# Optimization experiments

Measured on AMD Instinct MI355X. Metric: run time of the kernel, lower is better.

The kernel has to match this reference:

```python
import jax, jax.numpy as jnp
import numpy as np


def recursive_fht(x):
    # Faithful vectorized version of the module's recursive butterfly FHT
    # (twiddle = cas(2*pi*n/N), no flipped-odd term, exactly as in the source).
    N = x.shape[-1]
    if N == 1:
        return x
    e = recursive_fht(x[..., ::2])
    o = recursive_fht(x[..., 1::2])
    n = jnp.arange(N // 2, dtype=x.dtype)
    t = jnp.cos(2 * jnp.pi * n / N) + jnp.sin(2 * jnp.pi * n / N)
    return jnp.concatenate([e + t * o, e - t * o], axis=-1)


def compl_mul1d(x1, x2):
    # x1: [B, i, modes], x2: [i, o, modes]; flips along axis 0 as in the source
    x1f = x1[::-1]
    x2f = x2[::-1]
    return 0.5 * (jnp.einsum('bix,iox->box', x1, x2)
                  - jnp.einsum('bix,iox->box', x1f, x2f)
                  + jnp.einsum('bix,iox->box', x1, x2f)
                  + jnp.einsum('bix,iox->box', x1f, x2))


def idht(X):
    # Inverse discrete Hartley transform via the cas matrix (DHT is an
    # involution up to 1/K). K = N//2+1 is not a power of 2, so a dense
    # transform is used. Compute-bound batched GEMM.
    K = X.shape[-1]
    n = jnp.arange(K, dtype=X.dtype)
    ang = 2.0 * jnp.pi * jnp.outer(n, n) / K
    cas = jnp.cos(ang) + jnp.sin(ang)  # [K, K]
    return jnp.einsum('bck,kn->bcn', X, cas) / K


def setup_inputs() -> dict:
    key = jax.random.key(0)
    k1, k2 = jax.random.split(key)
    B, Cin, Cout, N, modes1 = 32, 64, 64, 4096, 1024
    x = jax.random.normal(k1, (B, Cin, N), dtype=jnp.float32)
    scale = 1.0 / (Cin * Cout)
    weights1 = scale * jax.random.uniform(k2, (Cin, Cout, modes1), dtype=jnp.float32)
    return {"x": x, "weights1": weights1, "modes1": modes1}


def reference(x, weights1, modes1):
    B, C, N = x.shape
    # dht with threshold=1.0: FHT along last axis, low-pass filter is a no-op
    x_ht = recursive_fht(x)
    K = N // 2 + 1
    out_ht = jnp.zeros((B, C, K), dtype=x.dtype)
    out_ht = out_ht.at[:, :, :modes1].set(compl_mul1d(x_ht[:, :, :modes1], weights1))
    return idht(out_ht)  # [B, C, N//2+1]
```

## Files before the change

kernel.cpp:

```cpp
#include <hip/hip_runtime.h>
#include <hip/hip_bf16.h>

#define BATCH 32
#define CIN   64
#define COUT  64
#define NFFT  4096
#define MODES 1024
#define KOUT  2049
#define NPAD  2176

typedef __bf16 bf16x8 __attribute__((ext_vector_type(8)));
typedef float  f32x4  __attribute__((ext_vector_type(4)));

#define AS1 __attribute__((address_space(1)))
#define AS3 __attribute__((address_space(3)))

static __device__ __forceinline__ void gl_lds16(const void* g, void* l) {
    __builtin_amdgcn_global_load_lds((const AS1 void*)g, (AS3 void*)l, 16, 0, 0);
}

static __device__ __forceinline__ void bfly4(float eA, float eB, float oA, float oB,
                                             float t, float c0, float c1,
                                             float& w0, float& w1, float& w2, float& w3) {
    float PA = fmaf(t, oA, eA), MA = fmaf(-t, oA, eA);
    float PB = fmaf(t, oB, eB), MB = fmaf(-t, oB, eB);
    w0 = fmaf(c0, PB, PA);
    w2 = fmaf(-c0, PB, PA);
    w1 = fmaf(c1, MB, MA);
    w3 = fmaf(-c1, MB, MA);
}


__global__ void fill_tw(float* __restrict__ tw) {
    int t = blockIdx.x * blockDim.x + threadIdx.x;
    if (t >= NFFT) return;
    if (t == 0) { tw[0] = 1.0f; return; }
    int h = 1 << (31 - __clz(t));
    int n = t - h;
    float ang = 3.14159265358979323846f * (float)n / (float)h;
    tw[t] = cosf(ang) + sinf(ang);
}

__global__ void fill_c2t(__hip_bfloat16* __restrict__ hi) {
    int idx = blockIdx.x * blockDim.x + threadIdx.x;
    if (idx >= NPAD * MODES) return;
    int n = idx >> 10;
    int k = idx & 1023;
    float v = 0.0f;
    if (n < KOUT) {
        int m = (k * n) % KOUT;
        float ang = 6.28318530717958647692f * (float)m / (float)KOUT;
        v = (cosf(ang) + sinf(ang)) * (1.0f / (float)KOUT);
    }
    hi[idx] = __float2bfloat16(v);
}

__global__ __launch_bounds__(256) void fht_kernel(const float* __restrict__ x,
                                                  const float* __restrict__ tw,
                                                  float* __restrict__ xh) {
    __shared__ float ldsA[4352];
    __shared__ float ldsB[4352];
    const int t = threadIdx.x;
    const int row = blockIdx.x;
    const float* xr = x + (size_t)row * NFFT;

    float r[4][4];
#pragma unroll
    for (int a = 0; a < 4; ++a)
#pragma unroll
        for (int c = 0; c < 4; ++c)
            r[a][c] = xr[t + 256 * a + 1024 * c];

    float o1[4][4];
#pragma unroll
    for (int a = 0; a < 4; ++a) {
        float PA = r[a][0] + r[a][2], MA = r[a][0] - r[a][2];
        float PB = r[a][1] + r[a][3], MB = r[a][1] - r[a][3];
        o1[a][0] = PA + PB;
        o1[a][2] = PA - PB;
        o1[a][1] = MA + MB;
        o1[a][3] = MA - MB;
    }
    float o2[4][4];
#pragma unroll
    for (int kap = 0; kap < 4; ++kap) {
        float tt = tw[4 + kap], c0 = tw[8 + kap], c1 = tw[12 + kap];
        bfly4(o1[0][kap], o1[1][kap], o1[2][kap], o1[3][kap], tt, c0, c1,
              o2[kap][0], o2[kap][1], o2[kap][2], o2[kap][3]);
    }
#pragma unroll
    for (int kap = 0; kap < 4; ++kap)
#pragma unroll
        for (int c = 0; c < 4; ++c) {
            int p = t + 256 * kap + 1024 * c;
            ldsA[p + (p >> 4)] = o2[kap][c];
        }
    __syncthreads();

    const int kap2 = t >> 4, gp = t & 15;
    float r2[4][4];
#pragma unroll
    for (int a = 0; a < 4; ++a)
#pragma unroll
        for (int c = 0; c < 4; ++c) {
            int p = 256 * kap2 + gp + 16 * a + 64 * c;
            r2[a][c] = ldsA[p + (p >> 4)];
        }
    float o3[4][4];
    {
        float tt = tw[16 + kap2], c0 = tw[32 + kap2], c1 = tw[48 + kap2];
#pragma unroll
        for (int a = 0; a < 4; ++a)
            bfly4(r2[a][0], r2[a][1], r2[a][2], r2[a][3], tt, c0, c1,
                  o3[a][0], o3[a][1], o3[a][2], o3[a][3]);
    }
    float o4[4][4];
#pragma unroll
    for (int c = 0; c < 4; ++c) {
        int kap3 = kap2 + 16 * c;
        float tt = tw[64 + kap3], c0 = tw[128 + kap3], c1 = tw[192 + kap3];
        bfly4(o3[0][c], o3[1][c], o3[2][c], o3[3][c], tt, c0, c1,
              o4[c][0], o4[c][1], o4[c][2], o4[c][3]);
    }
#pragma unroll
    for (int c = 0; c < 4; ++c)
#pragma unroll
        for (int cc = 0; cc < 4; ++cc) {
            int p = t + 256 * c + 1024 * cc;
            ldsB[p + (p >> 4)] = o4[c][cc];
        }
    __syncthreads();

    float r3[4][4];
#pragma unroll
    for (int g = 0; g < 4; ++g)
#pragma unroll
        for (int c = 0; c < 4; ++c) {
            int p = 16 * t + g + 4 * c;
            r3[g][c] = ldsB[p + (p >> 4)];
        }
    float o5[4][4];
    {
        float tt = tw[256 + t], c0 = tw[512 + t], c1 = tw[768 + t];
#pragma unroll
        for (int g = 0; g < 4; ++g)
            bfly4(r3[g][0], r3[g][1], r3[g][2], r3[g][3], tt, c0, c1,
                  o5[g][0], o5[g][1], o5[g][2], o5[g][3]);
    }
    float* xo = xh + (size_t)row * MODES;
#pragma unroll
    for (int c = 0; c < 4; ++c) {
        float tt = tw[1024 + t + 256 * c];
        float c0 = tw[2048 + t + 256 * c];
        float PA = fmaf(tt, o5[2][c], o5[0][c]);
        float PB = fmaf(tt, o5[3][c], o5[1][c]);
        xo[t + 256 * c] = fmaf(c0, PB, PA);
    }
}

__global__ __launch_bounds__(256) void mix_kernel(const f32x4* __restrict__ xh,
                                                  const f32x4* __restrict__ w,
                                                  ushort4* __restrict__ y_hi) {
    const int kl = threadIdx.x & 63;
    const int jg = threadIdx.x >> 6;
    const int k4 = blockIdx.x * 64 + kl;
    const int b  = blockIdx.y;
    const int rb = (BATCH - 1) - b;
    const int o  = blockIdx.z * 4 + jg;

    f32x4 accb = (f32x4){0.f, 0.f, 0.f, 0.f};
    f32x4 accr = (f32x4){0.f, 0.f, 0.f, 0.f};

#pragma unroll 4
    for (int i = 0; i < 32; ++i) {
        const int mi = 63 - i;
        f32x4 xai = xh[(size_t)(b  * CIN + i ) * 256 + k4];
        f32x4 xam = xh[(size_t)(b  * CIN + mi) * 256 + k4];
        f32x4 xbi = xh[(size_t)(rb * CIN + i ) * 256 + k4];
        f32x4 xbm = xh[(size_t)(rb * CIN + mi) * 256 + k4];
        f32x4 w1 = w[(size_t)(i  * COUT + o) * 256 + k4];
        f32x4 w2 = w[(size_t)(mi * COUT + o) * 256 + k4];
        f32x4 sa = xai + xam;
        f32x4 da = xai - xam;
        f32x4 sb = xbi + xbm;
        f32x4 db = xbi - xbm;
        f32x4 wp = w1 + w2, wm = w1 - w2;
        accb += sa * wp + db * wm;
        accr += sb * wp + da * wm;
    }

    const size_t ib = (size_t)(b  * COUT + o) * 256 + k4;
    const size_t ir = (size_t)(rb * COUT + o) * 256 + k4;
    f32x4 vb = accb * 0.5f;
    f32x4 vr = accr * 0.5f;
    __hip_bfloat16 b0 = __float2bfloat16(vb.x), b1 = __float2bfloat16(vb.y),
                   b2 = __float2bfloat16(vb.z), b3 = __float2bfloat16(vb.w);
    __hip_bfloat16 r0 = __float2bfloat16(vr.x), r1 = __float2bfloat16(vr.y),
                   r2 = __float2bfloat16(vr.z), r3 = __float2bfloat16(vr.w);
    y_hi[ib] = make_ushort4(*(unsigned short*)&b0, *(unsigned short*)&b1,
                            *(unsigned short*)&b2, *(unsigned short*)&b3);
    y_hi[ir] = make_ushort4(*(unsigned short*)&r0, *(unsigned short*)&r1,
                            *(unsigned short*)&r2, *(unsigned short*)&r3);
}

__global__ __launch_bounds__(256) void idht_mfma(const __hip_bfloat16* __restrict__ yh,
                                                 const __hip_bfloat16* __restrict__ ch,
                                                 float* __restrict__ out) {
    __shared__ __align__(16) char sa[2][8 * 1024];
    __shared__ __align__(16) char sb[2][4 * 1024];

    const int tid  = threadIdx.x;
    const int lane = tid & 63;
    const int wave = tid >> 6;
    const int wm = wave & 1;
    const int wn = wave >> 1;
    const int rbase = blockIdx.x * 128;
    const int nbase = blockIdx.y * 64;

    const int lrow = (lane & 15) * 2048;
    const int lchk = (lane >> 4) * 16;

    const char* ga  = (const char*)yh + (size_t)rbase * 2048;
    const char* gbh = (const char*)ch + (size_t)nbase * 2048;

    f32x4 acc[4][2];
#pragma unroll
    for (int mt = 0; mt < 4; ++mt)
#pragma unroll
        for (int nt = 0; nt < 2; ++nt) acc[mt][nt] = (f32x4){0.f, 0.f, 0.f, 0.f};

    auto stage = [&](int bi, int k0) {
#pragma unroll
        for (int r = 0; r < 2; ++r) {
            int g = wave + r * 4;
            gl_lds16(ga + (size_t)(g * 16) * 2048 + lrow + lchk + k0 * 2,
                     sa[bi] + g * 1024);
        }
        gl_lds16(gbh + (size_t)(wave * 16) * 2048 + lrow + lchk + k0 * 2,
                 sb[bi] + wave * 1024);
    };

    stage(0, 0);
    int cur = 0;
    for (int ks = 0; ks < MODES / 32; ++ks) {
        __syncthreads();
        if (ks + 1 < MODES / 32) stage(cur ^ 1, (ks + 1) * 32);
        bf16x8 a_[4], b_[2];
#pragma unroll
        for (int mt = 0; mt < 4; ++mt)
            a_[mt] = *(const bf16x8*)(sa[cur] + (wm * 4 + mt) * 1024 + lane * 16);
#pragma unroll
        for (int nt = 0; nt < 2; ++nt)
            b_[nt] = *(const bf16x8*)(sb[cur] + (wn * 2 + nt) * 1024 + lane * 16);
#pragma unroll
        for (int mt = 0; mt < 4; ++mt)
#pragma unroll
            for (int nt = 0; nt < 2; ++nt)
                acc[mt][nt] = __builtin_amdgcn_mfma_f32_16x16x32_bf16(a_[mt], b_[nt], acc[mt][nt], 0, 0, 0);
        cur ^= 1;
    }

#pragma unroll
    for (int mt = 0; mt < 4; ++mt) {
        int row = rbase + wm * 64 + mt * 16 + (lane >> 4) * 4;
#pragma unroll
        for (int nt = 0; nt < 2; ++nt) {
            int col = nbase + wn * 32 + nt * 16 + (lane & 15);
            if (col < KOUT) {
#pragma unroll
                for (int r = 0; r < 4; ++r)
                    out[(size_t)(row + r) * KOUT + col] = acc[mt][nt][r];
            }
        }
    }
}

extern "C" void kernel_launch(void* const* d_in, const int* in_sizes, int n_in,
                              void* d_out, int out_size, void* d_ws, size_t ws_size,
                              hipStream_t stream) {
    const float* x = (const float*)d_in[0];
    const float* w = (const float*)d_in[1];
    float* out = (float*)d_out;

    float* tw = (float*)d_ws;
    float* xh = tw + NFFT;
    __hip_bfloat16* y_hi = (__hip_bfloat16*)(xh + (size_t)BATCH * CIN * MODES);
    __hip_bfloat16* c2h  = y_hi + (size_t)BATCH * COUT * MODES;

    fill_tw<<<NFFT / 256, 256, 0, stream>>>(tw);
    fill_c2t<<<(NPAD * MODES + 255) / 256, 256, 0, stream>>>(c2h);
    fht_kernel<<<BATCH * CIN, 256, 0, stream>>>(x, tw, xh);
    mix_kernel<<<dim3(4, 16, 16), 256, 0, stream>>>((const f32x4*)xh, (const f32x4*)w,
                                                    (ushort4*)y_hi);
    idht_mfma<<<dim3((BATCH * COUT) / 128, NPAD / 64), 256, 0, stream>>>(y_hi, c2h, out);
}
```

Before: 161.0 us.

## Pre-swizzle cas table into MFMA fragment layout and load B directly to registers

The cas table is now written in a per-lane MFMA fragment order, so the idht kernel reads B straight from global memory into registers with one-step prefetch instead of staging it through LDS. The GEMM tile changes from 128x64 with 4 waves to 64x64 with 2 waves, and padding shrinks from 2176 to 2112 columns to cut wasted MFMA work. The two table-fill kernels are merged into one launch. In exchange, B is no longer shared through LDS between waves, so global/L2 traffic for the table rises and register pressure from the prefetch grows.

After: 154.0 us. -4.3%, faster.

```diff
diff --git a/kernel.cpp b/kernel.cpp
--- a/kernel.cpp
+++ b/kernel.cpp
@@ -7,7 +7,7 @@
 #define NFFT  4096
 #define MODES 1024
 #define KOUT  2049
-#define NPAD  2176
+#define NPAD  2112
 
 typedef __bf16 bf16x8 __attribute__((ext_vector_type(8)));
 typedef float  f32x4  __attribute__((ext_vector_type(4)));
@@ -30,29 +30,45 @@
     w3 = fmaf(-c1, MB, MA);
 }
 
-
-__global__ void fill_tw(float* __restrict__ tw) {
-    int t = blockIdx.x * blockDim.x + threadIdx.x;
-    if (t >= NFFT) return;
-    if (t == 0) { tw[0] = 1.0f; return; }
-    int h = 1 << (31 - __clz(t));
-    int n = t - h;
-    float ang = 3.14159265358979323846f * (float)n / (float)h;
-    tw[t] = cosf(ang) + sinf(ang);
-}
-
-__global__ void fill_c2t(__hip_bfloat16* __restrict__ hi) {
-    int idx = blockIdx.x * blockDim.x + threadIdx.x;
-    if (idx >= NPAD * MODES) return;
-    int n = idx >> 10;
-    int k = idx & 1023;
-    float v = 0.0f;
-    if (n < KOUT) {
-        int m = (k * n) % KOUT;
-        float ang = 6.28318530717958647692f * (float)m / (float)KOUT;
-        v = (cosf(ang) + sinf(ang)) * (1.0f / (float)KOUT);
-    }
-    hi[idx] = __float2bfloat16(v);
+#define NCHUNK ((NPAD / 16) * (MODES / 32) * 64)
+
+__global__ void fill_tables(float* __restrict__ tw, __hip_bfloat16* __restrict__ c2f) {
+    int gid = blockIdx.x * 256 + threadIdx.x;
+    if (gid < NCHUNK) {
+        int nl  = gid & 15;
+        int kc  = (gid >> 4) & 3;
+        int blk = gid >> 6;
+        int kb  = blk & 31;
+        int gn  = blk >> 5;
+        int n = gn * 16 + nl;
+        int kbase = kb * 32 + kc * 8;
+        unsigned short v8[8];
+        if (n < KOUT) {
+#pragma unroll
+            for (int j = 0; j < 8; ++j) {
+                int k = kbase + j;
+                int m = (k * n) % KOUT;
+                float ang = 6.28318530717958647692f * (float)m / (float)KOUT;
+                float v = (cosf(ang) + sinf(ang)) * (1.0f / (float)KOUT);
+                __hip_bfloat16 h = __float2bfloat16(v);
+                v8[j] = *(unsigned short*)&h;
+            }
+        } else {
+#pragma unroll
+            for (int j = 0; j < 8; ++j) v8[j] = 0;
+        }
+        *(ushort4*)((char*)c2f + (size_t)gid * 16)     = make_ushort4(v8[0], v8[1], v8[2], v8[3]);
+        *(ushort4*)((char*)c2f + (size_t)gid * 16 + 8) = make_ushort4(v8[4], v8[5], v8[6], v8[7]);
+    } else {
+        int t = gid - NCHUNK;
+        if (t < NFFT) {
+            if (t == 0) { tw[0] = 1.0f; return; }
+            int h = 1 << (31 - __clz(t));
+            int n = t - h;
+            float ang = 3.14159265358979323846f * (float)n / (float)h;
+            tw[t] = cosf(ang) + sinf(ang);
+        }
+    }
 }
 
 __global__ __launch_bounds__(256) void fht_kernel(const float* __restrict__ x,
@@ -203,69 +219,76 @@
                             *(unsigned short*)&r2, *(unsigned short*)&r3);
 }
 
-__global__ __launch_bounds__(256) void idht_mfma(const __hip_bfloat16* __restrict__ yh,
-                                                 const __hip_bfloat16* __restrict__ ch,
+__global__ __launch_bounds__(128) void idht_mfma(const __hip_bfloat16* __restrict__ yh,
+                                                 const __hip_bfloat16* __restrict__ c2f,
                                                  float* __restrict__ out) {
-    __shared__ __align__(16) char sa[2][8 * 1024];
-    __shared__ __align__(16) char sb[2][4 * 1024];
+    __shared__ __align__(16) char sa[2][4 * 1024];
 
     const int tid  = threadIdx.x;
     const int lane = tid & 63;
     const int wave = tid >> 6;
-    const int wm = wave & 1;
-    const int wn = wave >> 1;
-    const int rbase = blockIdx.x * 128;
-    const int nbase = blockIdx.y * 64;
+    const int rbase = blockIdx.x * 64;
+    const int gn0   = blockIdx.y * 4;
+    const int nbase = gn0 * 16;
 
     const int lrow = (lane & 15) * 2048;
     const int lchk = (lane >> 4) * 16;
 
-    const char* ga  = (const char*)yh + (size_t)rbase * 2048;
-    const char* gbh = (const char*)ch + (size_t)nbase * 2048;
-
-    f32x4 acc[4][2];
-#pragma unroll
-    for (int mt = 0; mt < 4; ++mt)
-#pragma unroll
-        for (int nt = 0; nt < 2; ++nt) acc[mt][nt] = (f32x4){0.f, 0.f, 0.f, 0.f};
-
-    auto stage = [&](int bi, int k0) {
+    const char* ga = (const char*)yh + (size_t)rbase * 2048;
+    const char* gb = (const char*)c2f;
+
+    f32x4 acc[2][4];
+#pragma unroll
+    for (int mt = 0; mt < 2; ++mt)
+#pragma unroll
+        for (int nt = 0; nt < 4; ++nt) acc[mt][nt] = (f32x4){0.f, 0.f, 0.f, 0.f};
+
+    auto stageA = [&](int bi, int k0) {
 #pragma unroll
         for (int r = 0; r < 2; ++r) {
-            int g = wave + r * 4;
+            int g = wave * 2 + r;
             gl_lds16(ga + (size_t)(g * 16) * 2048 + lrow + lchk + k0 * 2,
                      sa[bi] + g * 1024);
         }
-        gl_lds16(gbh + (size_t)(wave * 16) * 2048 + lrow + lchk + k0 * 2,
-                 sb[bi] + wave * 1024);
     };
-
-    stage(0, 0);
+    auto loadB = [&](int ks, bf16x8* b_) {
+#pragma unroll
+        for (int nt = 0; nt < 4; ++nt) {
+            size_t ch = ((size_t)(gn0 + nt) * 32 + ks) * 64 + lane;
+            b_[nt] = *(const bf16x8*)(gb + ch * 16);
+        }
+    };
+
+    stageA(0, 0);
+    bf16x8 bcur[4];
+    loadB(0, bcur);
     int cur = 0;
     for (int ks = 0; ks < MODES / 32; ++ks) {
         __syncthreads();
-        if (ks + 1 < MODES / 32) stage(cur ^ 1, (ks + 1) * 32);
-        bf16x8 a_[4], b_[2];
-#pragma unroll
-        for (int mt = 0; mt < 4; ++mt)
-            a_[mt] = *(const bf16x8*)(sa[cur] + (wm * 4 + mt) * 1024 + lane * 16);
-#pragma unroll
-        for (int nt = 0; nt < 2; ++nt)
-            b_[nt] = *(const bf16x8*)(sb[cur] + (wn * 2 + nt) * 1024 + lane * 16);
-#pragma unroll
-        for (int mt = 0; mt < 4; ++mt)
-#pragma unroll
-            for (int nt = 0; nt < 2; ++nt)
-                acc[mt][nt] = __builtin_amdgcn_mfma_f32_16x16x32_bf16(a_[mt], b_[nt], acc[mt][nt], 0, 0, 0);
+        if (ks + 1 < MODES / 32) stageA(cur ^ 1, (ks + 1) * 32);
+        bf16x8 bnext[4];
+        int kn = (ks + 1 < MODES / 32) ? ks + 1 : ks;
+        loadB(kn, bnext);
+        bf16x8 a_[2];
+#pragma unroll
+        for (int mt = 0; mt < 2; ++mt)
+            a_[mt] = *(const bf16x8*)(sa[cur] + (wave * 2 + mt) * 1024 + lane * 16);
+#pragma unroll
+        for (int mt = 0; mt < 2; ++mt)
+#pragma unroll
+            for (int nt = 0; nt < 4; ++nt)
+                acc[mt][nt] = __builtin_amdgcn_mfma_f32_16x16x32_bf16(a_[mt], bcur[nt], acc[mt][nt], 0, 0, 0);
+#pragma unroll
+        for (int nt = 0; nt < 4; ++nt) bcur[nt] = bnext[nt];
         cur ^= 1;
     }
 
 #pragma unroll
-    for (int mt = 0; mt < 4; ++mt) {
-        int row = rbase + wm * 64 + mt * 16 + (lane >> 4) * 4;
-#pragma unroll
-        for (int nt = 0; nt < 2; ++nt) {
-            int col = nbase + wn * 32 + nt * 16 + (lane & 15);
+    for (int mt = 0; mt < 2; ++mt) {
+        int row = rbase + wave * 32 + mt * 16 + (lane >> 4) * 4;
+#pragma unroll
+        for (int nt = 0; nt < 4; ++nt) {
+            int col = nbase + nt * 16 + (lane & 15);
             if (col < KOUT) {
 #pragma unroll
                 for (int r = 0; r < 4; ++r)
@@ -285,12 +308,11 @@
     float* tw = (float*)d_ws;
     float* xh = tw + NFFT;
     __hip_bfloat16* y_hi = (__hip_bfloat16*)(xh + (size_t)BATCH * CIN * MODES);
-    __hip_bfloat16* c2h  = y_hi + (size_t)BATCH * COUT * MODES;
-
-    fill_tw<<<NFFT / 256, 256, 0, stream>>>(tw);
-    fill_c2t<<<(NPAD * MODES + 255) / 256, 256, 0, stream>>>(c2h);
+    __hip_bfloat16* c2f  = y_hi + (size_t)BATCH * COUT * MODES;
+
+    fill_tables<<<(NCHUNK + NFFT + 255) / 256, 256, 0, stream>>>(tw, c2f);
     fht_kernel<<<BATCH * CIN, 256, 0, stream>>>(x, tw, xh);
     mix_kernel<<<dim3(4, 16, 16), 256, 0, stream>>>((const f32x4*)xh, (const f32x4*)w,
                                                     (ushort4*)y_hi);
-    idht_mfma<<<dim3((BATCH * COUT) / 128, NPAD / 64), 256, 0, stream>>>(y_hi, c2h, out);
-}
+    idht_mfma<<<dim3((BATCH * COUT) / 64, NPAD / 64), 128, 0, stream>>>(y_hi, c2f, out);
+}
```
